# Optimization experiments

Measured on AMD Instinct MI355X. Metric: run time of the kernel, lower is better.

Reference implementation:

```python
import jax, jax.numpy as jnp
import numpy as np

IMG_W = 256; IMG_H = 256; N_PTS = 320
MIN_DEPTH = 3.0; MAX_DEPTH = 9.0
NDC_EXTENT = 1.0; SCALING = 0.1; EPS = 1e-10


def setup_inputs() -> dict:
    key = jax.random.key(0)
    k1, k2, k3 = jax.random.split(key, 3)
    B, S = 1, 256
    image3d = jax.random.uniform(k1, (B, 1, S, S, S), dtype=jnp.float32)
    # random proper rotation via QR
    A = jax.random.normal(k2, (B, 3, 3), dtype=jnp.float32)
    Q, _ = jnp.linalg.qr(A)
    det = jnp.linalg.det(Q)
    R = Q * det[:, None, None]  # det(+1) for 3x3
    # camera ~6 world units in front of volume center (depth range 3..9)
    T = jnp.concatenate([0.1 * jax.random.normal(k3, (B, 2), dtype=jnp.float32),
                         jnp.full((B, 1), 6.0, jnp.float32)], axis=1)
    focal = jnp.full((B,), 4.0, jnp.float32)
    return {"image3d": image3d, "R": R, "T": T, "focal": focal}


def _trilinear(vol, pts):
    # vol: (C,D,H,W); pts: (N,3) xyz local coords in [-1,1]
    # grid_sample semantics: trilinear, align_corners=True, zero padding
    C, D, H, W = vol.shape
    gx = (pts[:, 0] + 1.0) * 0.5 * (W - 1)
    gy = (pts[:, 1] + 1.0) * 0.5 * (H - 1)
    gz = (pts[:, 2] + 1.0) * 0.5 * (D - 1)
    x0 = jnp.floor(gx); y0 = jnp.floor(gy); z0 = jnp.floor(gz)
    fx = gx - x0; fy = gy - y0; fz = gz - z0
    vol_flat = vol.reshape(C, D * H * W)
    out = jnp.zeros((C, pts.shape[0]), vol.dtype)
    for dz in (0, 1):
        wz = fz if dz else 1.0 - fz
        cz = z0 + dz
        for dy in (0, 1):
            wy = fy if dy else 1.0 - fy
            cy = y0 + dy
            for dx in (0, 1):
                wx = fx if dx else 1.0 - fx
                cx = x0 + dx
                valid = ((cx >= 0) & (cx <= W - 1) & (cy >= 0) & (cy <= H - 1)
                         & (cz >= 0) & (cz <= D - 1)).astype(vol.dtype)
                idx = ((jnp.clip(cz, 0, D - 1) * H + jnp.clip(cy, 0, H - 1)) * W
                       + jnp.clip(cx, 0, W - 1)).astype(jnp.int32)
                w = wx * wy * wz * valid
                out = out + vol_flat[:, idx] * w[None, :]
    return out


def _render(image3d, R, T, focal):
    B, C, D, H, W = image3d.shape
    voxel_size = 2.0 * NDC_EXTENT / max(C, D)  # shape = max(C, D) in original
    # Volumes local<->world scale per axis (pytorch3d): voxel_size*(size-1)/2
    scale = jnp.array([voxel_size * (W - 1) / 2.0,
                       voxel_size * (H - 1) / 2.0,
                       voxel_size * (D - 1) / 2.0], jnp.float32)
    # NDCMultinomialRaysampler pixel grid (pytorch3d: +x left, +y up, decreasing)
    xs = jnp.linspace(1.0 - 1.0 / IMG_W, -1.0 + 1.0 / IMG_W, IMG_W)
    ys = jnp.linspace(1.0 - 1.0 / IMG_H, -1.0 + 1.0 / IMG_H, IMG_H)
    depths = jnp.linspace(MIN_DEPTH, MAX_DEPTH, N_PTS).astype(jnp.float32)
    gy, gx = jnp.meshgrid(ys, xs, indexing="ij")  # (Hi,Wi)

    # channel 0: gray volume (features); channel 1: ones (density support)
    vol2 = jnp.concatenate([image3d[:, :1], jnp.ones_like(image3d[:, :1])], axis=1)

    def one(volC, Rb, Tb, fb):
        # unproject NDC pixels at each depth: cam pt = (x*d/f, y*d/f, d)
        cx = gx[:, :, None] * depths[None, None, :] / fb
        cy = gy[:, :, None] * depths[None, None, :] / fb
        cz = jnp.broadcast_to(depths, (IMG_H, IMG_W, N_PTS))
        cam = jnp.stack([cx, cy, cz], -1).reshape(-1, 3)       # (N,3)
        world = (cam - Tb) @ Rb.T                              # X_view = X_world @ R + T
        local = world / scale
        return _trilinear(volC, local)                          # (2,N)

    samp = jax.vmap(one)(vol2, R, T, focal)                     # (B,2,N)
    samp = samp.reshape(B, 2, IMG_H, IMG_W, N_PTS)
    gray = samp[:, 0]
    dens = SCALING * samp[:, 1]

    # EmissionAbsorptionRaymarcher (shifted cumprod, shift=1)
    cp = jnp.cumprod((1.0 + EPS) - dens, axis=-1)
    absorption = jnp.concatenate([jnp.ones_like(cp[..., :1]), cp[..., :-1]], axis=-1)
    weights = dens * absorption
    feat = jnp.sum(weights * gray, axis=-1)                     # RGB channels are equal
    opacity = 1.0 - jnp.prod(1.0 - dens, axis=-1)

    # RGBA (B,Hi,Wi,4) -> permute(0,3,2,1) -> mean over channel = (3*feat+alpha)/4
    screen = (3.0 * feat + opacity) / 4.0
    screen = jnp.transpose(screen, (0, 2, 1))[:, None]          # (B,1,Wi,Hi)

    # norm_type='standardized': normalized(standardized(x)), torch std is unbiased
    s = (screen - screen.mean()) / (jnp.std(screen, ddof=1) + 1e-8)
    return (s - s.min() + 1e-8) / (s.max() - s.min() + 1e-8)


def reference(image3d, R, T, focal):
    return _render(image3d, R, T, focal)
```

## Files before the change

### kernel.cpp

```cpp
#include <hip/hip_runtime.h>
#include <math.h>

#define IMG    256
#define NPTS   320
#define CHUNKS 8
#define SPC    40
#define NBLK   1024

__global__ __launch_bounds__(512)
void xray_render(const float* __restrict__ vol,
                 const float* __restrict__ Rm,
                 const float* __restrict__ Tv,
                 const float* __restrict__ fc,
                 float* __restrict__ outv,
                 float* __restrict__ partials)
{
    const int tid = threadIdx.x;
    const int p   = tid & 63;
    const int c   = tid >> 6;
    const int w   = (blockIdx.x << 3) + (p & 7);
    const int h   = (blockIdx.y << 3) + (p >> 3);

    const float f   = fc[0];
    const float r00 = Rm[0], r01 = Rm[1], r02 = Rm[2];
    const float r10 = Rm[3], r11 = Rm[4], r12 = Rm[5];
    const float r20 = Rm[6], r21 = Rm[7], r22 = Rm[8];
    const float t0  = Tv[0], t1  = Tv[1], t2  = Tv[2];

    const float invf = 1.0f / f;
    const float px = 0.99609375f - (float)w * 0.0078125f;
    const float py = 0.99609375f - (float)h * 0.0078125f;
    const float dcx = px * invf, dcy = py * invf;

    const float dwx = r00*dcx + r01*dcy + r02;
    const float dwy = r10*dcx + r11*dcy + r12;
    const float dwz = r20*dcx + r21*dcy + r22;
    const float ox  = -(r00*t0 + r01*t1 + r02*t2);
    const float oy  = -(r10*t0 + r11*t1 + r12*t2);
    const float oz  = -(r20*t0 + r21*t1 + r22*t2);

    const float g0x = fmaf(384.0f, dwx, fmaf(128.0f, ox, 127.5f));
    const float g0y = fmaf(384.0f, dwy, fmaf(128.0f, oy, 127.5f));
    const float g0z = fmaf(384.0f, dwz, fmaf(128.0f, oz, 127.5f));
    const float K   = 768.0f / 319.0f;
    const float gsx = K*dwx, gsy = K*dwy, gsz = K*dwz;

    float raylo = -1e30f, rayhi = 1e30f;
    {
        const float g0a[3] = {g0x, g0y, g0z};
        const float gsa[3] = {gsx, gsy, gsz};
        #pragma unroll
        for (int a = 0; a < 3; ++a) {
            if (fabsf(gsa[a]) > 1e-9f) {
                float u = (-1.0f  - g0a[a]) / gsa[a];
                float v = (256.0f - g0a[a]) / gsa[a];
                raylo = fmaxf(raylo, fminf(u, v));
                rayhi = fminf(rayhi, fmaxf(u, v));
            } else if (!(g0a[a] > -1.0f && g0a[a] < 256.0f)) {
                raylo = 1e30f; rayhi = -1e30f;
            }
        }
    }
    float a0 = fmaxf(raylo - 1.0f, (float)(c * SPC));
    float a1 = fminf(rayhi + 1.0f, (float)(c * SPC + SPC - 1));
    a0 = fminf(fmaxf(a0, 0.0f),  400.0f);
    a1 = fminf(fmaxf(a1, -1.0f), 400.0f);
    const int i0 = (int)ceilf(a0);
    const int i1 = (int)floorf(a1);

    float feat = 0.0f, Tc = 1.0f, pr = 1.0f;

    for (int i = i0; i <= i1; ++i) {
        const float fi = (float)i;
        const float gx = fmaf(fi, gsx, g0x);
        const float gy = fmaf(fi, gsy, g0y);
        const float gz = fmaf(fi, gsz, g0z);
        const float xf = floorf(gx), yf = floorf(gy), zf = floorf(gz);
        const float fx = gx - xf, fy = gy - yf, fz = gz - zf;
        const int ix = (int)xf, iy = (int)yf, iz = (int)zf;

        if ((unsigned)ix <= 254u && (unsigned)iy <= 254u && (unsigned)iz <= 254u) {
            const float* b = vol + ((iz << 16) + (iy << 8) + ix);
            const float v000 = b[0],     v001 = b[1];
            const float v010 = b[256],   v011 = b[257];
            const float v100 = b[65536], v101 = b[65537];
            const float v110 = b[65792], v111 = b[65793];
            const float c00 = fmaf(fx, v001 - v000, v000);
            const float c01 = fmaf(fx, v011 - v010, v010);
            const float c10 = fmaf(fx, v101 - v100, v100);
            const float c11 = fmaf(fx, v111 - v110, v110);
            const float c0  = fmaf(fy, c01 - c00, c00);
            const float c1  = fmaf(fy, c11 - c10, c10);
            const float gray = fmaf(fz, c1 - c0, c0);
            feat = fmaf(0.1f * Tc, gray, feat);
            Tc *= 0.9f;
            pr *= 0.9f;
        } else {
            const float wx0 = (ix >= 0  && ix <= 255) ? (1.0f - fx) : 0.0f;
            const float wx1 = (ix >= -1 && ix <= 254) ? fx          : 0.0f;
            const float wy0 = (iy >= 0  && iy <= 255) ? (1.0f - fy) : 0.0f;
            const float wy1 = (iy >= -1 && iy <= 254) ? fy          : 0.0f;
            const float wz0 = (iz >= 0  && iz <= 255) ? (1.0f - fz) : 0.0f;
            const float wz1 = (iz >= -1 && iz <= 254) ? fz          : 0.0f;
            const float cov = (wx0 + wx1) * (wy0 + wy1) * (wz0 + wz1);
            if (cov > 0.0f) {
                const int x0 = min(max(ix, 0), 255),   x1 = min(max(ix + 1, 0), 255);
                const int y0 = min(max(iy, 0), 255),   y1 = min(max(iy + 1, 0), 255);
                const int z0 = min(max(iz, 0), 255),   z1 = min(max(iz + 1, 0), 255);
                const float* bz0 = vol + (z0 << 16);
                const float* bz1 = vol + (z1 << 16);
                const int ry0 = y0 << 8, ry1 = y1 << 8;
                const float s0 = (bz0[ry0 + x0]*wx0 + bz0[ry0 + x1]*wx1) * wy0
                               + (bz0[ry1 + x0]*wx0 + bz0[ry1 + x1]*wx1) * wy1;
                const float s1 = (bz1[ry0 + x0]*wx0 + bz1[ry0 + x1]*wx1) * wy0
                               + (bz1[ry1 + x0]*wx0 + bz1[ry1 + x1]*wx1) * wy1;
                const float gray = s0 * wz0 + s1 * wz1;
                const float dens = 0.1f * cov;
                feat = fmaf(dens * Tc, gray, feat);
                const float m = 1.0f - dens;
                Tc *= m;
                pr *= m;
            }
        }
    }

    __shared__ float sf[CHUNKS][64];
    __shared__ float sT[CHUNKS][64];
    __shared__ float sp[CHUNKS][64];
    sf[c][p] = feat; sT[c][p] = Tc; sp[c][p] = pr;
    __syncthreads();

    if (tid < 64) {
        float F = sf[CHUNKS - 1][p];
        #pragma unroll
        for (int j = CHUNKS - 2; j >= 0; --j) F = fmaf(sT[j][p], F, sf[j][p]);
        float PR = sp[0][p];
        #pragma unroll
        for (int j = 1; j < CHUNKS; ++j) PR *= sp[j][p];

        const float screen = fmaf(3.0f, F, 1.0f - PR) * 0.25f;
        outv[(w << 8) + h] = screen;

        float s = screen, s2 = screen * screen, mn = screen, mx = screen;
        #pragma unroll
        for (int o = 32; o; o >>= 1) {
            s  += __shfl_xor(s,  o);
            s2 += __shfl_xor(s2, o);
            mn  = fminf(mn, __shfl_xor(mn, o));
            mx  = fmaxf(mx, __shfl_xor(mx, o));
        }
        if (p == 0) {
            const int bid = (blockIdx.y << 5) + blockIdx.x;
            partials[bid * 4 + 0] = s;
            partials[bid * 4 + 1] = s2;
            partials[bid * 4 + 2] = mn;
            partials[bid * 4 + 3] = mx;
        }
    }
}

__global__ __launch_bounds__(256)
void xray_finalize(const float* __restrict__ partials, float* __restrict__ scal)
{
    const int t = threadIdx.x;
    double s = 0.0, s2 = 0.0;
    float mn = 1e30f, mx = -1e30f;
    for (int j = t; j < NBLK; j += 256) {
        s  += (double)partials[j * 4 + 0];
        s2 += (double)partials[j * 4 + 1];
        mn  = fminf(mn, partials[j * 4 + 2]);
        mx  = fmaxf(mx, partials[j * 4 + 3]);
    }
    for (int o = 32; o; o >>= 1) {
        s  += __shfl_xor(s,  o);
        s2 += __shfl_xor(s2, o);
        mn  = fminf(mn, __shfl_xor(mn, o));
        mx  = fmaxf(mx, __shfl_xor(mx, o));
    }
    __shared__ double ls[4], ls2[4];
    __shared__ float  lmn[4], lmx[4];
    const int wid = t >> 6, lane = t & 63;
    if (lane == 0) { ls[wid] = s; ls2[wid] = s2; lmn[wid] = mn; lmx[wid] = mx; }
    __syncthreads();
    if (t == 0) {
        const double S  = ls[0] + ls[1] + ls[2] + ls[3];
        const double S2 = ls2[0] + ls2[1] + ls2[2] + ls2[3];
        const float MN = fminf(fminf(lmn[0], lmn[1]), fminf(lmn[2], lmn[3]));
        const float MX = fmaxf(fmaxf(lmx[0], lmx[1]), fmaxf(lmx[2], lmx[3]));
        const double N   = 65536.0;
        double var = (S2 - S * S / N) / (N - 1.0);
        if (var < 0.0) var = 0.0;
        const double sdp = sqrt(var) + 1e-8;
        const float off = MN - (float)(1e-8 * sdp);
        const float inv = 1.0f / (MX - off);
        scal[0] = off;
        scal[1] = inv;
    }
}

__global__ __launch_bounds__(256)
void xray_normalize(float* __restrict__ outv, const float* __restrict__ scal)
{
    const int i = blockIdx.x * 256 + threadIdx.x;
    const float off = scal[0], inv = scal[1];
    outv[i] = (outv[i] - off) * inv;
}

extern "C" void kernel_launch(void* const* d_in, const int* in_sizes, int n_in,
                              void* d_out, int out_size, void* d_ws, size_t ws_size,
                              hipStream_t stream)
{
    const float* vol = (const float*)d_in[0];
    const float* Rm  = (const float*)d_in[1];
    const float* Tv  = (const float*)d_in[2];
    const float* fc  = (const float*)d_in[3];
    float* outv = (float*)d_out;
    float* partials = (float*)d_ws;
    float* scal = partials + 4 * NBLK;

    dim3 grid(IMG / 8, IMG / 8);
    xray_render<<<grid, 512, 0, stream>>>(vol, Rm, Tv, fc, outv, partials);
    xray_finalize<<<1, 256, 0, stream>>>(partials, scal);
    xray_normalize<<<256, 256, 0, stream>>>(outv, scal);
}
```

Before: 66.33 us.

## Split ray loop into analytic interior span and boundary steps; fuse finalize into normalize

Each ray's sample range is split analytically into a fully-interior span, which runs a branch-free unrolled trilinear loop, and boundary prefix and suffix segments that use the general zero-padded sampler. The separate product accumulator is dropped because it equals the transmittance Tc. The single-block finalize kernel is merged into the normalize kernel, so every block redundantly reduces the 1024 partials, removing one launch. This trades some redundant reduction work and more code size for less divergence in the inner loop and fewer kernel launches.

After: 73.61 us. +11.0%, slower.

```diff
diff --git a/kernel.cpp b/kernel.cpp
--- a/kernel.cpp
+++ b/kernel.cpp
@@ -46,31 +46,43 @@
     const float gsx = K*dwx, gsy = K*dwy, gsz = K*dwz;
 
     float raylo = -1e30f, rayhi = 1e30f;
+    float inlo  = -1e30f, inhi  = 1e30f;
     {
         const float g0a[3] = {g0x, g0y, g0z};
         const float gsa[3] = {gsx, gsy, gsz};
         #pragma unroll
         for (int a = 0; a < 3; ++a) {
-            if (fabsf(gsa[a]) > 1e-9f) {
-                float u = (-1.0f  - g0a[a]) / gsa[a];
-                float v = (256.0f - g0a[a]) / gsa[a];
+            const float g0 = g0a[a], gs = gsa[a];
+            if (fabsf(gs) > 1e-6f) {
+                const float r = 1.0f / gs;
+                const float u = (-1.0f  - g0) * r;
+                const float v = (256.0f - g0) * r;
                 raylo = fmaxf(raylo, fminf(u, v));
                 rayhi = fminf(rayhi, fmaxf(u, v));
-            } else if (!(g0a[a] > -1.0f && g0a[a] < 256.0f)) {
-                raylo = 1e30f; rayhi = -1e30f;
+                const float s = (0.001f   - g0) * r;
+                const float t = (254.999f - g0) * r;
+                inlo = fmaxf(inlo, fminf(s, t));
+                inhi = fminf(inhi, fmaxf(s, t));
+            } else {
+                if (!(g0 > -1.0f && g0 < 256.0f))        { raylo = 1e30f; rayhi = -1e30f; }
+                if (!(g0 > 0.001f && g0 < 254.999f))     { inlo  = 1e30f; inhi  = -1e30f; }
             }
         }
     }
-    float a0 = fmaxf(raylo - 1.0f, (float)(c * SPC));
-    float a1 = fminf(rayhi + 1.0f, (float)(c * SPC + SPC - 1));
-    a0 = fminf(fmaxf(a0, 0.0f),  400.0f);
-    a1 = fminf(fmaxf(a1, -1.0f), 400.0f);
+    const float c0f = (float)(c * SPC);
+    const float c1f = c0f + (float)(SPC - 1);
+    float a0 = fminf(fmaxf(fmaxf(raylo - 1.0f, c0f), 0.0f),  400.0f);
+    float a1 = fminf(fmaxf(fminf(rayhi + 1.0f, c1f), -1.0f), 400.0f);
     const int i0 = (int)ceilf(a0);
     const int i1 = (int)floorf(a1);
-
-    float feat = 0.0f, Tc = 1.0f, pr = 1.0f;
-
-    for (int i = i0; i <= i1; ++i) {
+    float b0 = fminf(fmaxf(inlo, (float)i0), 401.0f);
+    float b1 = fmaxf(fminf(inhi, (float)i1), -2.0f);
+    const int jLo = (int)ceilf(b0);
+    const int jHi = (int)floorf(b1);
+
+    float feat = 0.0f, Tc = 1.0f;
+
+    auto bstep = [&](int i) {
         const float fi = (float)i;
         const float gx = fmaf(fi, gsx, g0x);
         const float gy = fmaf(fi, gsy, g0y);
@@ -78,8 +90,46 @@
         const float xf = floorf(gx), yf = floorf(gy), zf = floorf(gz);
         const float fx = gx - xf, fy = gy - yf, fz = gz - zf;
         const int ix = (int)xf, iy = (int)yf, iz = (int)zf;
-
-        if ((unsigned)ix <= 254u && (unsigned)iy <= 254u && (unsigned)iz <= 254u) {
+        const float wx0 = (ix >= 0  && ix <= 255) ? (1.0f - fx) : 0.0f;
+        const float wx1 = (ix >= -1 && ix <= 254) ? fx          : 0.0f;
+        const float wy0 = (iy >= 0  && iy <= 255) ? (1.0f - fy) : 0.0f;
+        const float wy1 = (iy >= -1 && iy <= 254) ? fy          : 0.0f;
+        const float wz0 = (iz >= 0  && iz <= 255) ? (1.0f - fz) : 0.0f;
+        const float wz1 = (iz >= -1 && iz <= 254) ? fz          : 0.0f;
+        const float cov = (wx0 + wx1) * (wy0 + wy1) * (wz0 + wz1);
+        if (cov > 0.0f) {
+            const int x0 = min(max(ix, 0), 255),   x1 = min(max(ix + 1, 0), 255);
+            const int y0 = min(max(iy, 0), 255),   y1 = min(max(iy + 1, 0), 255);
+            const int z0 = min(max(iz, 0), 255),   z1 = min(max(iz + 1, 0), 255);
+            const float* bz0 = vol + (z0 << 16);
+            const float* bz1 = vol + (z1 << 16);
+            const int ry0 = y0 << 8, ry1 = y1 << 8;
+            const float s0 = (bz0[ry0 + x0]*wx0 + bz0[ry0 + x1]*wx1) * wy0
+                           + (bz0[ry1 + x0]*wx0 + bz0[ry1 + x1]*wx1) * wy1;
+            const float s1 = (bz1[ry0 + x0]*wx0 + bz1[ry0 + x1]*wx1) * wy0
+                           + (bz1[ry1 + x0]*wx0 + bz1[ry1 + x1]*wx1) * wy1;
+            const float gray = s0 * wz0 + s1 * wz1;
+            const float dens = 0.1f * cov;
+            feat = fmaf(dens * Tc, gray, feat);
+            Tc *= (1.0f - dens);
+        }
+    };
+
+    if (jLo <= jHi) {
+        for (int i = i0; i < jLo; ++i) bstep(i);
+
+        #pragma unroll 4
+        for (int i = jLo; i <= jHi; ++i) {
+            const float fi = (float)i;
+            const float gx = fmaf(fi, gsx, g0x);
+            const float gy = fmaf(fi, gsy, g0y);
+            const float gz = fmaf(fi, gsz, g0z);
+            const int ix = (int)gx;
+            const int iy = (int)gy;
+            const int iz = (int)gz;
+            const float fx = gx - (float)ix;
+            const float fy = gy - (float)iy;
+            const float fz = gz - (float)iz;
             const float* b = vol + ((iz << 16) + (iy << 8) + ix);
             const float v000 = b[0],     v001 = b[1];
             const float v010 = b[256],   v011 = b[257];
@@ -89,54 +139,30 @@
             const float c01 = fmaf(fx, v011 - v010, v010);
             const float c10 = fmaf(fx, v101 - v100, v100);
             const float c11 = fmaf(fx, v111 - v110, v110);
-            const float c0  = fmaf(fy, c01 - c00, c00);
-            const float c1  = fmaf(fy, c11 - c10, c10);
-            const float gray = fmaf(fz, c1 - c0, c0);
+            const float d0  = fmaf(fy, c01 - c00, c00);
+            const float d1  = fmaf(fy, c11 - c10, c10);
+            const float gray = fmaf(fz, d1 - d0, d0);
             feat = fmaf(0.1f * Tc, gray, feat);
             Tc *= 0.9f;
-            pr *= 0.9f;
-        } else {
-            const float wx0 = (ix >= 0  && ix <= 255) ? (1.0f - fx) : 0.0f;
-            const float wx1 = (ix >= -1 && ix <= 254) ? fx          : 0.0f;
-            const float wy0 = (iy >= 0  && iy <= 255) ? (1.0f - fy) : 0.0f;
-            const float wy1 = (iy >= -1 && iy <= 254) ? fy          : 0.0f;
-            const float wz0 = (iz >= 0  && iz <= 255) ? (1.0f - fz) : 0.0f;
-            const float wz1 = (iz >= -1 && iz <= 254) ? fz          : 0.0f;
-            const float cov = (wx0 + wx1) * (wy0 + wy1) * (wz0 + wz1);
-            if (cov > 0.0f) {
-                const int x0 = min(max(ix, 0), 255),   x1 = min(max(ix + 1, 0), 255);
-                const int y0 = min(max(iy, 0), 255),   y1 = min(max(iy + 1, 0), 255);
-                const int z0 = min(max(iz, 0), 255),   z1 = min(max(iz + 1, 0), 255);
-                const float* bz0 = vol + (z0 << 16);
-                const float* bz1 = vol + (z1 << 16);
-                const int ry0 = y0 << 8, ry1 = y1 << 8;
-                const float s0 = (bz0[ry0 + x0]*wx0 + bz0[ry0 + x1]*wx1) * wy0
-                               + (bz0[ry1 + x0]*wx0 + bz0[ry1 + x1]*wx1) * wy1;
-                const float s1 = (bz1[ry0 + x0]*wx0 + bz1[ry0 + x1]*wx1) * wy0
-                               + (bz1[ry1 + x0]*wx0 + bz1[ry1 + x1]*wx1) * wy1;
-                const float gray = s0 * wz0 + s1 * wz1;
-                const float dens = 0.1f * cov;
-                feat = fmaf(dens * Tc, gray, feat);
-                const float m = 1.0f - dens;
-                Tc *= m;
-                pr *= m;
-            }
-        }
+        }
+
+        for (int i = jHi + 1; i <= i1; ++i) bstep(i);
+    } else {
+        for (int i = i0; i <= i1; ++i) bstep(i);
     }
 
     __shared__ float sf[CHUNKS][64];
     __shared__ float sT[CHUNKS][64];
-    __shared__ float sp[CHUNKS][64];
-    sf[c][p] = feat; sT[c][p] = Tc; sp[c][p] = pr;
+    sf[c][p] = feat; sT[c][p] = Tc;
     __syncthreads();
 
     if (tid < 64) {
         float F = sf[CHUNKS - 1][p];
         #pragma unroll
         for (int j = CHUNKS - 2; j >= 0; --j) F = fmaf(sT[j][p], F, sf[j][p]);
-        float PR = sp[0][p];
-        #pragma unroll
-        for (int j = 1; j < CHUNKS; ++j) PR *= sp[j][p];
+        float PR = sT[0][p];
+        #pragma unroll
+        for (int j = 1; j < CHUNKS; ++j) PR *= sT[j][p];
 
         const float screen = fmaf(3.0f, F, 1.0f - PR) * 0.25f;
         outv[(w << 8) + h] = screen;
@@ -160,17 +186,20 @@
 }
 
 __global__ __launch_bounds__(256)
-void xray_finalize(const float* __restrict__ partials, float* __restrict__ scal)
+void xray_normalize(float* __restrict__ outv, const float* __restrict__ partials)
 {
     const int t = threadIdx.x;
     double s = 0.0, s2 = 0.0;
     float mn = 1e30f, mx = -1e30f;
-    for (int j = t; j < NBLK; j += 256) {
-        s  += (double)partials[j * 4 + 0];
-        s2 += (double)partials[j * 4 + 1];
-        mn  = fminf(mn, partials[j * 4 + 2]);
-        mx  = fmaxf(mx, partials[j * 4 + 3]);
-    }
+    #pragma unroll
+    for (int j = 0; j < NBLK / 256; ++j) {
+        const int idx = (j * 256 + t) * 4;
+        s  += (double)partials[idx + 0];
+        s2 += (double)partials[idx + 1];
+        mn  = fminf(mn, partials[idx + 2]);
+        mx  = fmaxf(mx, partials[idx + 3]);
+    }
+    #pragma unroll
     for (int o = 32; o; o >>= 1) {
         s  += __shfl_xor(s,  o);
         s2 += __shfl_xor(s2, o);
@@ -179,6 +208,7 @@
     }
     __shared__ double ls[4], ls2[4];
     __shared__ float  lmn[4], lmx[4];
+    __shared__ float  soff, sinv;
     const int wid = t >> 6, lane = t & 63;
     if (lane == 0) { ls[wid] = s; ls2[wid] = s2; lmn[wid] = mn; lmx[wid] = mx; }
     __syncthreads();
@@ -187,23 +217,16 @@
         const double S2 = ls2[0] + ls2[1] + ls2[2] + ls2[3];
         const float MN = fminf(fminf(lmn[0], lmn[1]), fminf(lmn[2], lmn[3]));
         const float MX = fmaxf(fmaxf(lmx[0], lmx[1]), fmaxf(lmx[2], lmx[3]));
-        const double N   = 65536.0;
-        double var = (S2 - S * S / N) / (N - 1.0);
+        double var = (S2 - S * S / 65536.0) / 65535.0;
         if (var < 0.0) var = 0.0;
         const double sdp = sqrt(var) + 1e-8;
         const float off = MN - (float)(1e-8 * sdp);
-        const float inv = 1.0f / (MX - off);
-        scal[0] = off;
-        scal[1] = inv;
-    }
-}
-
-__global__ __launch_bounds__(256)
-void xray_normalize(float* __restrict__ outv, const float* __restrict__ scal)
-{
-    const int i = blockIdx.x * 256 + threadIdx.x;
-    const float off = scal[0], inv = scal[1];
-    outv[i] = (outv[i] - off) * inv;
+        soff = off;
+        sinv = 1.0f / (MX - off);
+    }
+    __syncthreads();
+    const int i = blockIdx.x * 256 + t;
+    outv[i] = (outv[i] - soff) * sinv;
 }
 
 extern "C" void kernel_launch(void* const* d_in, const int* in_sizes, int n_in,
@@ -216,10 +239,8 @@
     const float* fc  = (const float*)d_in[3];
     float* outv = (float*)d_out;
     float* partials = (float*)d_ws;
-    float* scal = partials + 4 * NBLK;
 
     dim3 grid(IMG / 8, IMG / 8);
     xray_render<<<grid, 512, 0, stream>>>(vol, Rm, Tv, fc, outv, partials);
-    xray_finalize<<<1, 256, 0, stream>>>(partials, scal);
-    xray_normalize<<<256, 256, 0, stream>>>(outv, scal);
+    xray_normalize<<<IMG * IMG / 256, 256, 0, stream>>>(outv, partials);
 }
```

## Split each ray's clipped range evenly across chunks and fuse finalize into normalize

Applied to the files above, without the earlier changes.

Each ray's active sample range is now clipped to the volume first and then divided evenly among 8 chunk threads, replacing the fixed 40-sample chunks. Previously many threads sat idle on empty chunks while others did all the work. Blocks shrink to 32 pixels × 8 chunks (256 threads, 2048 blocks), and the separate transmittance product is dropped because it equals the product of chunk Tc values. The finalize kernel is merged into normalize, with every block redundantly reducing all 2048 partials, which saves a launch at the cost of duplicated reduction work.

Measured after the change: 74.46 us. +12.3%, slower.

```diff
diff --git a/kernel.cpp b/kernel.cpp
--- a/kernel.cpp
+++ b/kernel.cpp
@@ -4,10 +4,10 @@
 #define IMG    256
 #define NPTS   320
 #define CHUNKS 8
-#define SPC    40
-#define NBLK   1024
-
-__global__ __launch_bounds__(512)
+#define PX     32
+#define NBLK   2048
+
+__global__ __launch_bounds__(256)
 void xray_render(const float* __restrict__ vol,
                  const float* __restrict__ Rm,
                  const float* __restrict__ Tv,
@@ -15,11 +15,15 @@
                  float* __restrict__ outv,
                  float* __restrict__ partials)
 {
+    const int bid = blockIdx.x;
+    const int bx  = bid & 31;
+    const int by  = bid >> 5;
+
     const int tid = threadIdx.x;
-    const int p   = tid & 63;
-    const int c   = tid >> 6;
-    const int w   = (blockIdx.x << 3) + (p & 7);
-    const int h   = (blockIdx.y << 3) + (p >> 3);
+    const int p   = tid & 31;
+    const int c   = tid >> 5;
+    const int w   = (bx << 3) + (p & 7);
+    const int h   = (by << 2) + (p >> 3);
 
     const float f   = fc[0];
     const float r00 = Rm[0], r01 = Rm[1], r02 = Rm[2];
@@ -61,16 +65,17 @@
             }
         }
     }
-    float a0 = fmaxf(raylo - 1.0f, (float)(c * SPC));
-    float a1 = fminf(rayhi + 1.0f, (float)(c * SPC + SPC - 1));
-    a0 = fminf(fmaxf(a0, 0.0f),  400.0f);
-    a1 = fminf(fmaxf(a1, -1.0f), 400.0f);
-    const int i0 = (int)ceilf(a0);
-    const int i1 = (int)floorf(a1);
-
-    float feat = 0.0f, Tc = 1.0f, pr = 1.0f;
-
-    for (int i = i0; i <= i1; ++i) {
+    float a0 = fminf(fmaxf(raylo - 1.0f, 0.0f),  400.0f);
+    float a1 = fminf(fmaxf(fminf(rayhi + 1.0f, (float)(NPTS - 1)), -1.0f), 400.0f);
+    const int i0  = (int)ceilf(a0);
+    const int i1  = (int)floorf(a1);
+    const int len = max(0, i1 - i0 + 1);
+    const int s0  = i0 + ((len * c) >> 3);
+    const int s1  = i0 + ((len * (c + 1)) >> 3) - 1;
+
+    float feat = 0.0f, Tc = 1.0f;
+
+    for (int i = s0; i <= s1; ++i) {
         const float fi = (float)i;
         const float gx = fmaf(fi, gsx, g0x);
         const float gy = fmaf(fi, gsy, g0y);
@@ -94,7 +99,6 @@
             const float gray = fmaf(fz, c1 - c0, c0);
             feat = fmaf(0.1f * Tc, gray, feat);
             Tc *= 0.9f;
-            pr *= 0.9f;
         } else {
             const float wx0 = (ix >= 0  && ix <= 255) ? (1.0f - fx) : 0.0f;
             const float wx1 = (ix >= -1 && ix <= 254) ? fx          : 0.0f;
@@ -110,67 +114,65 @@
                 const float* bz0 = vol + (z0 << 16);
                 const float* bz1 = vol + (z1 << 16);
                 const int ry0 = y0 << 8, ry1 = y1 << 8;
-                const float s0 = (bz0[ry0 + x0]*wx0 + bz0[ry0 + x1]*wx1) * wy0
-                               + (bz0[ry1 + x0]*wx0 + bz0[ry1 + x1]*wx1) * wy1;
-                const float s1 = (bz1[ry0 + x0]*wx0 + bz1[ry0 + x1]*wx1) * wy0
-                               + (bz1[ry1 + x0]*wx0 + bz1[ry1 + x1]*wx1) * wy1;
-                const float gray = s0 * wz0 + s1 * wz1;
+                const float sv0 = (bz0[ry0 + x0]*wx0 + bz0[ry0 + x1]*wx1) * wy0
+                                + (bz0[ry1 + x0]*wx0 + bz0[ry1 + x1]*wx1) * wy1;
+                const float sv1 = (bz1[ry0 + x0]*wx0 + bz1[ry0 + x1]*wx1) * wy0
+                                + (bz1[ry1 + x0]*wx0 + bz1[ry1 + x1]*wx1) * wy1;
+                const float gray = sv0 * wz0 + sv1 * wz1;
                 const float dens = 0.1f * cov;
                 feat = fmaf(dens * Tc, gray, feat);
-                const float m = 1.0f - dens;
-                Tc *= m;
-                pr *= m;
+                Tc *= (1.0f - dens);
             }
         }
     }
 
-    __shared__ float sf[CHUNKS][64];
-    __shared__ float sT[CHUNKS][64];
-    __shared__ float sp[CHUNKS][64];
-    sf[c][p] = feat; sT[c][p] = Tc; sp[c][p] = pr;
+    __shared__ float sf[CHUNKS][PX];
+    __shared__ float sT[CHUNKS][PX];
+    sf[c][p] = feat; sT[c][p] = Tc;
     __syncthreads();
 
-    if (tid < 64) {
+    if (tid < PX) {
         float F = sf[CHUNKS - 1][p];
         #pragma unroll
         for (int j = CHUNKS - 2; j >= 0; --j) F = fmaf(sT[j][p], F, sf[j][p]);
-        float PR = sp[0][p];
-        #pragma unroll
-        for (int j = 1; j < CHUNKS; ++j) PR *= sp[j][p];
+        float PR = sT[0][p];
+        #pragma unroll
+        for (int j = 1; j < CHUNKS; ++j) PR *= sT[j][p];
 
         const float screen = fmaf(3.0f, F, 1.0f - PR) * 0.25f;
         outv[(w << 8) + h] = screen;
 
         float s = screen, s2 = screen * screen, mn = screen, mx = screen;
         #pragma unroll
-        for (int o = 32; o; o >>= 1) {
+        for (int o = 16; o; o >>= 1) {
             s  += __shfl_xor(s,  o);
             s2 += __shfl_xor(s2, o);
             mn  = fminf(mn, __shfl_xor(mn, o));
             mx  = fmaxf(mx, __shfl_xor(mx, o));
         }
         if (p == 0) {
-            const int bid = (blockIdx.y << 5) + blockIdx.x;
-            partials[bid * 4 + 0] = s;
-            partials[bid * 4 + 1] = s2;
-            partials[bid * 4 + 2] = mn;
-            partials[bid * 4 + 3] = mx;
+            float4* out4 = (float4*)partials;
+            out4[bid] = make_float4(s, s2, mn, mx);
         }
     }
 }
 
 __global__ __launch_bounds__(256)
-void xray_finalize(const float* __restrict__ partials, float* __restrict__ scal)
+void xray_normalize(float* __restrict__ outv, const float* __restrict__ partials)
 {
     const int t = threadIdx.x;
+    const float4* p4 = (const float4*)partials;
     double s = 0.0, s2 = 0.0;
     float mn = 1e30f, mx = -1e30f;
-    for (int j = t; j < NBLK; j += 256) {
-        s  += (double)partials[j * 4 + 0];
-        s2 += (double)partials[j * 4 + 1];
-        mn  = fminf(mn, partials[j * 4 + 2]);
-        mx  = fmaxf(mx, partials[j * 4 + 3]);
-    }
+    #pragma unroll
+    for (int j = 0; j < NBLK / 256; ++j) {
+        const float4 v = p4[j * 256 + t];
+        s  += (double)v.x;
+        s2 += (double)v.y;
+        mn  = fminf(mn, v.z);
+        mx  = fmaxf(mx, v.w);
+    }
+    #pragma unroll
     for (int o = 32; o; o >>= 1) {
         s  += __shfl_xor(s,  o);
         s2 += __shfl_xor(s2, o);
@@ -179,6 +181,7 @@
     }
     __shared__ double ls[4], ls2[4];
     __shared__ float  lmn[4], lmx[4];
+    __shared__ float  soff, sinv;
     const int wid = t >> 6, lane = t & 63;
     if (lane == 0) { ls[wid] = s; ls2[wid] = s2; lmn[wid] = mn; lmx[wid] = mx; }
     __syncthreads();
@@ -187,23 +190,16 @@
         const double S2 = ls2[0] + ls2[1] + ls2[2] + ls2[3];
         const float MN = fminf(fminf(lmn[0], lmn[1]), fminf(lmn[2], lmn[3]));
         const float MX = fmaxf(fmaxf(lmx[0], lmx[1]), fmaxf(lmx[2], lmx[3]));
-        const double N   = 65536.0;
-        double var = (S2 - S * S / N) / (N - 1.0);
+        double var = (S2 - S * S / 65536.0) / 65535.0;
         if (var < 0.0) var = 0.0;
         const double sdp = sqrt(var) + 1e-8;
         const float off = MN - (float)(1e-8 * sdp);
-        const float inv = 1.0f / (MX - off);
-        scal[0] = off;
-        scal[1] = inv;
-    }
-}
-
-__global__ __launch_bounds__(256)
-void xray_normalize(float* __restrict__ outv, const float* __restrict__ scal)
-{
-    const int i = blockIdx.x * 256 + threadIdx.x;
-    const float off = scal[0], inv = scal[1];
-    outv[i] = (outv[i] - off) * inv;
+        soff = off;
+        sinv = 1.0f / (MX - off);
+    }
+    __syncthreads();
+    const int i = blockIdx.x * 256 + t;
+    outv[i] = (outv[i] - soff) * sinv;
 }
 
 extern "C" void kernel_launch(void* const* d_in, const int* in_sizes, int n_in,
@@ -216,10 +212,7 @@
     const float* fc  = (const float*)d_in[3];
     float* outv = (float*)d_out;
     float* partials = (float*)d_ws;
-    float* scal = partials + 4 * NBLK;
-
-    dim3 grid(IMG / 8, IMG / 8);
-    xray_render<<<grid, 512, 0, stream>>>(vol, Rm, Tv, fc, outv, partials);
-    xray_finalize<<<1, 256, 0, stream>>>(partials, scal);
-    xray_normalize<<<256, 256, 0, stream>>>(outv, scal);
+
+    xray_render<<<NBLK, 256, 0, stream>>>(vol, Rm, Tv, fc, outv, partials);
+    xray_normalize<<<IMG * IMG / 256, 256, 0, stream>>>(outv, partials);
 }
```
